# Kernel optimization log

Hardware: AMD Instinct MI355X
Metric: run time of the kernel (lower is better)

Reference implementation:

```python
import jax, jax.numpy as jnp
import numpy as np
import math

N = 512
H = 512
L = 16384
R_MIN, R_MAX, MAX_PHASE = 0.0, 1.0, 6.283


def setup_inputs() -> dict:
    key = jax.random.key(0)
    ks = jax.random.split(key, 8)
    u1 = jax.random.uniform(ks[0], (N,))
    u2 = jax.random.uniform(ks[1], (N,))
    nu_log = jnp.log(-0.5 * jnp.log(u1 * (R_MAX ** 2 - R_MIN ** 2) + R_MIN ** 2))
    theta_log = jnp.log(u2 * MAX_PHASE)
    B_re = jax.random.normal(ks[2], (N, H)) / math.sqrt(2 * H)
    B_im = jax.random.normal(ks[3], (N, H)) / math.sqrt(2 * H)
    C_re = jax.random.normal(ks[4], (H, N)) / math.sqrt(N)
    C_im = jax.random.normal(ks[5], (H, N)) / math.sqrt(N)
    D = jax.random.normal(ks[6], (H,))
    diag_lambda = jnp.exp(-jnp.exp(nu_log) + 1j * jnp.exp(theta_log))
    gamma_log = jnp.log(jnp.sqrt(1.0 - jnp.abs(diag_lambda) ** 2))
    x = jax.random.normal(ks[7], (L, H), dtype=jnp.float32)
    # state is Lambda's multiplier in the original code; ones => standard LRU
    state_re = jnp.ones((N,), dtype=jnp.float32)
    state_im = jnp.zeros((N,), dtype=jnp.float32)
    return {"x": x, "state_re": state_re, "state_im": state_im,
            "nu_log": nu_log, "theta_log": theta_log, "gamma_log": gamma_log,
            "B_re": B_re, "B_im": B_im, "C_re": C_re, "C_im": C_im, "D": D}


def _binop(ei, ej):
    a_i, bu_i = ei
    a_j, bu_j = ej
    return (a_j * a_i, a_j * bu_i + bu_j)


def reference(x, state_re, state_im, nu_log, theta_log, gamma_log,
              B_re, B_im, C_re, C_im, D):
    Lambda = jnp.exp(-jnp.exp(nu_log) + 1j * jnp.exp(theta_log))  # (N,) c64
    # NOTE: original uses exp(i*gamma_log) (a phase), faithful here
    exp_gamma = jnp.exp(1j * gamma_log.astype(jnp.complex64))      # (N,)
    B = (B_re + 1j * B_im) * exp_gamma[:, None]                    # (N,H)
    C = C_re + 1j * C_im                                           # (H,N)
    state = state_re + 1j * state_im                               # (N,)
    a0 = Lambda * state                                            # (N,)
    a_elems = jnp.broadcast_to(a0, (x.shape[0], a0.shape[0]))      # (L,N)
    xc = x.astype(jnp.complex64)                                   # (L,H)
    Bu = xc @ B.T                                                  # (L,N)
    _, inner_states = jax.lax.associative_scan(_binop, (a_elems, Bu))
    y = jnp.real(inner_states @ C.T) + D[None, :] * x              # (L,H)
    return y
```

## Files before the change

### kernel.cpp

```cpp
#include <hip/hip_runtime.h>
#include <hip/hip_bf16.h>
#include <cstdint>

#define L_SEQ 16384
#define NST   512
#define HDIM  512
#define CH    512
#define CT    32

typedef __attribute__((ext_vector_type(8))) short short8;
typedef __attribute__((ext_vector_type(4))) float f32x4;

static __device__ __forceinline__ ushort f2bf(float f) {
  union { float f; unsigned int u; } v; v.f = f;
  unsigned int r = v.u + 0x7fffu + ((v.u >> 16) & 1u);
  return (ushort)(r >> 16);
}
static __device__ __forceinline__ float bf2f(ushort u) {
  union { unsigned int u; float f; } v; v.u = ((unsigned int)u) << 16;
  return v.f;
}

static __device__ __forceinline__ void mfma_16x16x32_bf16(f32x4& d, short8 a, short8 b) {
  asm("v_mfma_f32_16x16x32_bf16 %0, %1, %2, %0" : "+v"(d) : "v"(a), "v"(b));
}

static __device__ __forceinline__ void gload_lds16(const ushort* g, ushort* l) {
  __builtin_amdgcn_global_load_lds((__attribute__((address_space(1))) void*)(g),
                                   (__attribute__((address_space(3))) void*)(l),
                                   16, 0, 0);
}


__global__ __launch_bounds__(256) void setup_all(
    const float* __restrict__ st_re, const float* __restrict__ st_im,
    const float* __restrict__ nu_log, const float* __restrict__ theta_log,
    const float* __restrict__ gamma_log,
    const float* __restrict__ B_re, const float* __restrict__ B_im,
    const float* __restrict__ C_re, const float* __restrict__ C_im,
    const float* __restrict__ X,
    float2* __restrict__ lam, float2* __restrict__ lamT,
    ushort* __restrict__ W1, ushort* __restrict__ W2,
    ushort* __restrict__ xb)
{
  int bid = blockIdx.x, tid = threadIdx.x;
  if (bid < 4096) {
    size_t i = ((size_t)bid * 256 + tid) * 8;
#pragma unroll
    for (int j = 0; j < 8; j += 4) {
      float4 v = *(const float4*)(X + i + j);
      ushort4 o;
      o.x = f2bf(v.x); o.y = f2bf(v.y); o.z = f2bf(v.z); o.w = f2bf(v.w);
      *(ushort4*)(xb + i + j) = o;
    }
  } else if (bid < 5120) {
    int idx = (bid - 4096) * 256 + tid;
    int n = idx >> 9, h = idx & 511;
    float g = gamma_log[n];
    float sg, cg; sincosf(g, &sg, &cg);
    float br = B_re[idx], bi = B_im[idx];
    W1[(size_t)(2 * n) * 512 + h]     = f2bf(br * cg - bi * sg);
    W1[(size_t)(2 * n + 1) * 512 + h] = f2bf(br * sg + bi * cg);
  } else if (bid < 6144) {
    int idx = (bid - 5120) * 256 + tid;
    int hh = idx >> 9, n = idx & 511;
    W2[(size_t)hh * 1024 + 2 * n]     = f2bf(C_re[idx]);
    W2[(size_t)hh * 1024 + 2 * n + 1] = f2bf(-C_im[idx]);
  } else {
    int n = (bid - 6144) * 256 + tid;
    float nu  = expf(nu_log[n]);
    float th  = expf(theta_log[n]);
    float mag = expf(-nu);
    float sth, cth; sincosf(th, &sth, &cth);
    float lr = mag * cth, li = mag * sth;
    float sr = st_re[n], si = st_im[n];
    float ar = lr * sr - li * si;
    float ai = lr * si + li * sr;
    lam[n] = make_float2(ar, ai);
    float pr = ar, pi = ai;
#pragma unroll
    for (int i = 0; i < 5; ++i) {
      float nr = pr * pr - pi * pi;
      float ni = 2.f * pr * pi;
      pr = nr; pi = ni;
    }
    lamT[n] = make_float2(pr, pi);
  }
}

template <int BM, int BN, int WMW, int WNW, int EPI>
__global__ __launch_bounds__(WMW * WNW * 64, 4)
void gemm_p(const ushort* __restrict__ A, const ushort* __restrict__ Bm,
            ushort* __restrict__ Cb, float* __restrict__ Cf,
            const float* __restrict__ Dv, const ushort* __restrict__ Xb,
            const float2* __restrict__ lam, float2* __restrict__ carry,
            int M, int Ncols, int K)
{
  constexpr int THREADS = WMW * WNW * 64;
  constexpr int FM = BM / (WMW * 16);
  constexpr int FN = BN / (WNW * 16);
  constexpr int SLOT = (BM + BN) * 32;
  constexpr int LPT  = (BM + BN) * 4 / THREADS;
  static_assert(LPT == 3 || LPT == 4, "vmcnt immediates cover LPT 3/4");
  static_assert(EPI != 0 || 3 * SLOT >= BM * BN, "ring must hold C-tile for LDS carries");
  __shared__ __align__(16) ushort lds[3 * SLOT];

  const int t = threadIdx.x, lane = t & 63, w = t >> 6;
  const int wr = w / WNW, wc = w % WNW;
  const int m0 = blockIdx.x * BM, n0 = blockIdx.y * BN;
  const int rr = lane & 15, kk = (lane >> 4) * 8;
  const int swzu = ((rr >> 1) & 3) << 3;
  const int NK = K / 32;

  f32x4 acc[FM][FN];
#pragma unroll
  for (int i = 0; i < FM; ++i)
#pragma unroll
    for (int j = 0; j < FN; ++j) { f32x4 z = {0.f, 0.f, 0.f, 0.f}; acc[i][j] = z; }

  auto stage = [&](int kt) {
    int k0 = kt * 32;
    ushort* base = lds + (kt % 3) * SLOT;
#pragma unroll
    for (int j = 0; j < LPT; ++j) {
      int d = j * THREADS + t;
      const ushort* g;
      if (d < BM * 4) {
        int row = d >> 2;
        int sl  = (d & 3) ^ ((row >> 1) & 3);
        g = A + (size_t)(m0 + row) * K + k0 + sl * 8;
      } else {
        int dd = d - BM * 4;
        int row = dd >> 2;
        int sl  = (dd & 3) ^ ((row >> 1) & 3);
        g = Bm + (size_t)(n0 + row) * K + k0 + sl * 8;
      }
      gload_lds16(g, base + d * 8);
    }
  };

  stage(0); stage(1);
  if constexpr (LPT == 4) asm volatile("s_waitcnt vmcnt(4)" ::: "memory");
  else                    asm volatile("s_waitcnt vmcnt(3)" ::: "memory");
  asm volatile("s_barrier" ::: "memory");

  for (int kt = 0; kt < NK; ++kt) {
    if (kt + 2 < NK) stage(kt + 2);
    const ushort* As = lds + (kt % 3) * SLOT;
    const ushort* Bs = As + BM * 32;
    short8 af[FM], bb[FN];
#pragma unroll
    for (int mi = 0; mi < FM; ++mi)
      af[mi] = *(const short8*)(As + (wr * FM * 16 + mi * 16 + rr) * 32 + (kk ^ swzu));
#pragma unroll
    for (int ni = 0; ni < FN; ++ni)
      bb[ni] = *(const short8*)(Bs + (wc * FN * 16 + ni * 16 + rr) * 32 + (kk ^ swzu));
    __builtin_amdgcn_s_setprio(1);
#pragma unroll
    for (int mi = 0; mi < FM; ++mi)
#pragma unroll
      for (int ni = 0; ni < FN; ++ni)
        mfma_16x16x32_bf16(acc[mi][ni], af[mi], bb[ni]);
    __builtin_amdgcn_s_setprio(0);
    if (kt <= NK - 3) {
      if constexpr (LPT == 4) asm volatile("s_waitcnt vmcnt(4)" ::: "memory");
      else                    asm volatile("s_waitcnt vmcnt(3)" ::: "memory");
    } else {
      asm volatile("s_waitcnt vmcnt(0)" ::: "memory");
    }
    asm volatile("s_barrier" ::: "memory");
  }

  const int crow = (lane >> 4) * 4, ccol = lane & 15;
#pragma unroll
  for (int mi = 0; mi < FM; ++mi) {
#pragma unroll
    for (int ni = 0; ni < FN; ++ni) {
      int col = n0 + wc * FN * 16 + ni * 16 + ccol;
#pragma unroll
      for (int r = 0; r < 4; ++r) {
        int row = m0 + wr * FM * 16 + mi * 16 + crow + r;
        float v = acc[mi][ni][r];
        size_t idx = (size_t)row * Ncols + col;
        if constexpr (EPI == 0) {
          ushort bv = f2bf(v);
          Cb[idx] = bv;
          lds[(row - m0) * BN + (col - n0)] = bv;
        } else {
          Cf[idx] = v + Dv[col] * bf2f(Xb[idx]);
        }
      }
    }
  }

  if constexpr (EPI == 0) {
    __syncthreads();
    {
      int c  = t >> 7;
      int ch = t & 127;
      float2 a = lam[(n0 >> 1) + ch];
      float cr = 0.f, ci = 0.f;
      const ushort* p = lds + (c * 32) * BN + 2 * ch;
#pragma unroll 8
      for (int r = 0; r < 32; ++r) {
        ushort2 v = *(const ushort2*)(p + r * BN);
        float br = bf2f(v.x), bi = bf2f(v.y);
        float nr = a.x * cr - a.y * ci + br;
        float ni = a.x * ci + a.y * cr + bi;
        cr = nr; ci = ni;
      }
      carry[(size_t)((n0 >> 1) + ch) * CH + (m0 >> 5) + c] = make_float2(cr, ci);
    }
  }
}

__global__ __launch_bounds__(CH) void scanC(const float2* __restrict__ carry,
                                            const float2* __restrict__ lamT,
                                            float2* __restrict__ prefix)
{
  int n = blockIdx.x;
  int c = threadIdx.x;
  __shared__ float2 buf[CH];
  float2 aT = lamT[n];
  float2 v = carry[(size_t)n * CH + c];
  buf[c] = v;
  __syncthreads();
  float mr = aT.x, mi = aT.y;
#pragma unroll
  for (int s = 1; s < CH; s <<= 1) {
    float2 o = make_float2(0.f, 0.f);
    if (c >= s) o = buf[c - s];
    __syncthreads();
    v.x += mr * o.x - mi * o.y;
    v.y += mr * o.y + mi * o.x;
    buf[c] = v;
    __syncthreads();
    float nmr = mr * mr - mi * mi;
    float nmi = 2.f * mr * mi;
    mr = nmr; mi = nmi;
  }
  float2 p = (c == 0) ? make_float2(0.f, 0.f) : buf[c - 1];
  prefix[(size_t)n * CH + c] = p;
}

__global__ __launch_bounds__(256) void scanB(ushort* __restrict__ Bu,
                                             const float2* __restrict__ lam,
                                             const float2* __restrict__ prefix)
{
  int b = blockIdx.x;
  int c = (b & ~63) | ((b & 7) << 3) | ((b >> 3) & 7);
  int q = threadIdx.x;
  float2 a0 = lam[2 * q], a1 = lam[2 * q + 1];
  float2 g0 = prefix[(size_t)(2 * q) * CH + c];
  float2 g1 = prefix[(size_t)(2 * q + 1) * CH + c];
  float hr0 = g0.x, hi0 = g0.y, hr1 = g1.x, hi1 = g1.y;
  ushort* base = Bu + (size_t)c * CT * 1024 + 4 * q;
#pragma unroll 4
  for (int tt = 0; tt < CT; ++tt) {
    ushort4 v = *(const ushort4*)(base + tt * 1024);
    float nr0 = a0.x * hr0 - a0.y * hi0 + bf2f(v.x);
    float ni0 = a0.x * hi0 + a0.y * hr0 + bf2f(v.y);
    hr0 = nr0; hi0 = ni0;
    float nr1 = a1.x * hr1 - a1.y * hi1 + bf2f(v.z);
    float ni1 = a1.x * hi1 + a1.y * hr1 + bf2f(v.w);
    hr1 = nr1; hi1 = ni1;
    ushort4 o;
    o.x = f2bf(hr0); o.y = f2bf(hi0);
    o.z = f2bf(hr1); o.w = f2bf(hi1);
    *(ushort4*)(base + tt * 1024) = o;
  }
}

extern "C" void kernel_launch(void* const* d_in, const int* in_sizes, int n_in,
                              void* d_out, int out_size, void* d_ws, size_t ws_size,
                              hipStream_t stream)
{
  const float* x         = (const float*)d_in[0];
  const float* state_re  = (const float*)d_in[1];
  const float* state_im  = (const float*)d_in[2];
  const float* nu_log    = (const float*)d_in[3];
  const float* theta_log = (const float*)d_in[4];
  const float* gamma_log = (const float*)d_in[5];
  const float* B_re      = (const float*)d_in[6];
  const float* B_im      = (const float*)d_in[7];
  const float* C_re      = (const float*)d_in[8];
  const float* C_im      = (const float*)d_in[9];
  const float* Dv        = (const float*)d_in[10];
  float* y = (float*)d_out;

  char* ws = (char*)d_ws;
  size_t off = 0;
  float2* lam    = (float2*)(ws + off); off += 4096;
  float2* lamT   = (float2*)(ws + off); off += 4096;
  float2* carry  = (float2*)(ws + off); off += (size_t)CH * NST * sizeof(float2);
  float2* prefix = (float2*)(ws + off); off += (size_t)CH * NST * sizeof(float2);
  ushort* W1 = (ushort*)(ws + off); off += (size_t)2 * NST * HDIM * sizeof(ushort);
  ushort* W2 = (ushort*)(ws + off); off += (size_t)HDIM * 2 * NST * sizeof(ushort);
  ushort* xb = (ushort*)(ws + off); off += (size_t)L_SEQ * HDIM * sizeof(ushort);
  ushort* Bu = (ushort*)(ws + off); off += (size_t)L_SEQ * 2 * NST * sizeof(ushort);

  setup_all<<<6146, 256, 0, stream>>>(state_re, state_im, nu_log, theta_log,
                                      gamma_log, B_re, B_im, C_re, C_im, x,
                                      lam, lamT, W1, W2, xb);

  gemm_p<128, 256, 2, 4, 0><<<dim3(L_SEQ / 128, (2 * NST) / 256), 512, 0, stream>>>(
      xb, W1, Bu, nullptr, nullptr, nullptr, lam, carry, L_SEQ, 2 * NST, HDIM);

  scanC<<<NST, CH, 0, stream>>>(carry, lamT, prefix);
  scanB<<<CH, 256, 0, stream>>>(Bu, lam, prefix);

  gemm_p<128, 256, 2, 4, 1><<<dim3(L_SEQ / 128, HDIM / 256), 512, 0, stream>>>(
      Bu, W2, nullptr, y, Dv, xb, nullptr, nullptr, L_SEQ, HDIM, 2 * NST);
}
```

Baseline: 80.62 us.

## Double GEMM K-tile depth to 64 with 8-way XOR swizzle and fewer barriers

Raises the K depth of each staged tile from 32 to 64, so each loop iteration does two MFMA sub-steps and there are half as many barrier/waitcnt synchronisations. The LDS layout switches to an 8-chunk XOR swizzle, and the LDS fragment reads are hoisted ahead of issuing the next global stage. In exchange, LDS use per block doubles and the occupancy hint in launch_bounds drops from 4 to 2, which may lower occupancy. The code now requires exactly 6 loads per thread per tile, which constrains which tile configurations are valid.

```diff
diff --git a/kernel.cpp b/kernel.cpp
--- a/kernel.cpp
+++ b/kernel.cpp
@@ -89,28 +89,31 @@
 }
 
 template <int BM, int BN, int WMW, int WNW, int EPI>
-__global__ __launch_bounds__(WMW * WNW * 64, 4)
+__global__ __launch_bounds__(WMW * WNW * 64, 2)
 void gemm_p(const ushort* __restrict__ A, const ushort* __restrict__ Bm,
             ushort* __restrict__ Cb, float* __restrict__ Cf,
             const float* __restrict__ Dv, const ushort* __restrict__ Xb,
             const float2* __restrict__ lam, float2* __restrict__ carry,
             int M, int Ncols, int K)
 {
+  constexpr int BK = 64;
   constexpr int THREADS = WMW * WNW * 64;
   constexpr int FM = BM / (WMW * 16);
   constexpr int FN = BN / (WNW * 16);
-  constexpr int SLOT = (BM + BN) * 32;
-  constexpr int LPT  = (BM + BN) * 4 / THREADS;
-  static_assert(LPT == 3 || LPT == 4, "vmcnt immediates cover LPT 3/4");
+  constexpr int GR = BK / 8;
+  constexpr int SLOT = (BM + BN) * BK;
+  constexpr int LPT  = (BM + BN) * GR / THREADS;
+  static_assert(LPT == 6, "vmcnt immediates assume 6 loads/thread/tile");
   static_assert(EPI != 0 || 3 * SLOT >= BM * BN, "ring must hold C-tile for LDS carries");
   __shared__ __align__(16) ushort lds[3 * SLOT];
 
   const int t = threadIdx.x, lane = t & 63, w = t >> 6;
   const int wr = w / WNW, wc = w % WNW;
   const int m0 = blockIdx.x * BM, n0 = blockIdx.y * BN;
-  const int rr = lane & 15, kk = (lane >> 4) * 8;
-  const int swzu = ((rr >> 1) & 3) << 3;
-  const int NK = K / 32;
+  const int rr = lane & 15;
+  const int g4 = lane >> 4;
+  const int swz3 = rr & 7;
+  const int NK = K / BK;
 
   f32x4 acc[FM][FN];
 #pragma unroll
@@ -119,20 +122,20 @@
     for (int j = 0; j < FN; ++j) { f32x4 z = {0.f, 0.f, 0.f, 0.f}; acc[i][j] = z; }
 
   auto stage = [&](int kt) {
-    int k0 = kt * 32;
+    int k0 = kt * BK;
     ushort* base = lds + (kt % 3) * SLOT;
 #pragma unroll
     for (int j = 0; j < LPT; ++j) {
       int d = j * THREADS + t;
       const ushort* g;
-      if (d < BM * 4) {
-        int row = d >> 2;
-        int sl  = (d & 3) ^ ((row >> 1) & 3);
+      if (d < BM * GR) {
+        int row = d >> 3;
+        int sl  = (d & 7) ^ (row & 7);
         g = A + (size_t)(m0 + row) * K + k0 + sl * 8;
       } else {
-        int dd = d - BM * 4;
-        int row = dd >> 2;
-        int sl  = (dd & 3) ^ ((row >> 1) & 3);
+        int dd = d - BM * GR;
+        int row = dd >> 3;
+        int sl  = (dd & 7) ^ (row & 7);
         g = Bm + (size_t)(n0 + row) * K + k0 + sl * 8;
       }
       gload_lds16(g, base + d * 8);
@@ -140,21 +143,24 @@
   };
 
   stage(0); stage(1);
-  if constexpr (LPT == 4) asm volatile("s_waitcnt vmcnt(4)" ::: "memory");
-  else                    asm volatile("s_waitcnt vmcnt(3)" ::: "memory");
+  asm volatile("s_waitcnt vmcnt(6)" ::: "memory");
   asm volatile("s_barrier" ::: "memory");
 
   for (int kt = 0; kt < NK; ++kt) {
+    const ushort* As = lds + (kt % 3) * SLOT;
+    const ushort* Bs = As + BM * BK;
+    short8 af[FM], bb[FN];
+#pragma unroll
+    for (int mi = 0; mi < FM; ++mi) {
+      int row = wr * FM * 16 + mi * 16 + rr;
+      af[mi] = *(const short8*)(As + row * BK + ((g4 ^ swz3) << 3));
+    }
+#pragma unroll
+    for (int ni = 0; ni < FN; ++ni) {
+      int row = wc * FN * 16 + ni * 16 + rr;
+      bb[ni] = *(const short8*)(Bs + row * BK + ((g4 ^ swz3) << 3));
+    }
     if (kt + 2 < NK) stage(kt + 2);
-    const ushort* As = lds + (kt % 3) * SLOT;
-    const ushort* Bs = As + BM * 32;
-    short8 af[FM], bb[FN];
-#pragma unroll
-    for (int mi = 0; mi < FM; ++mi)
-      af[mi] = *(const short8*)(As + (wr * FM * 16 + mi * 16 + rr) * 32 + (kk ^ swzu));
-#pragma unroll
-    for (int ni = 0; ni < FN; ++ni)
-      bb[ni] = *(const short8*)(Bs + (wc * FN * 16 + ni * 16 + rr) * 32 + (kk ^ swzu));
     __builtin_amdgcn_s_setprio(1);
 #pragma unroll
     for (int mi = 0; mi < FM; ++mi)
@@ -162,12 +168,26 @@
       for (int ni = 0; ni < FN; ++ni)
         mfma_16x16x32_bf16(acc[mi][ni], af[mi], bb[ni]);
     __builtin_amdgcn_s_setprio(0);
-    if (kt <= NK - 3) {
-      if constexpr (LPT == 4) asm volatile("s_waitcnt vmcnt(4)" ::: "memory");
-      else                    asm volatile("s_waitcnt vmcnt(3)" ::: "memory");
-    } else {
-      asm volatile("s_waitcnt vmcnt(0)" ::: "memory");
-    }
+    short8 af1[FM], bb1[FN];
+#pragma unroll
+    for (int mi = 0; mi < FM; ++mi) {
+      int row = wr * FM * 16 + mi * 16 + rr;
+      af1[mi] = *(const short8*)(As + row * BK + (((4 + g4) ^ swz3) << 3));
+    }
+#pragma unroll
+    for (int ni = 0; ni < FN; ++ni) {
+      int row = wc * FN * 16 + ni * 16 + rr;
+      bb1[ni] = *(const short8*)(Bs + row * BK + (((4 + g4) ^ swz3) << 3));
+    }
+    __builtin_amdgcn_s_setprio(1);
+#pragma unroll
+    for (int mi = 0; mi < FM; ++mi)
+#pragma unroll
+      for (int ni = 0; ni < FN; ++ni)
+        mfma_16x16x32_bf16(acc[mi][ni], af1[mi], bb1[ni]);
+    __builtin_amdgcn_s_setprio(0);
+    if (kt <= NK - 3) asm volatile("s_waitcnt vmcnt(6)" ::: "memory");
+    else              asm volatile("s_waitcnt vmcnt(0)" ::: "memory");
     asm volatile("s_barrier" ::: "memory");
   }
 
```

After: 80.81 us. Within noise of the previous version (+0.2%).
